# Kernel optimization log

Measured on AMD Instinct MI355X. Metric: run time of the kernel, lower is better.

## Reference

```python
import jax, jax.numpy as jnp
import numpy as np

B, F, V, E, H, D = 1024, 2048, 10000, 256, 512, 3


def setup_inputs() -> dict:
    key = jax.random.key(0)
    ks = jax.random.split(key, 16)
    n = lambda k, shape, s: (jax.random.normal(k, shape, dtype=jnp.float32) * s)
    fz = lambda shape: jnp.zeros(shape, jnp.float32)
    forget_bias = fz((4 * H,)).at[H:2 * H].set(1.0)  # torch init: bias_hh forget gate = 1
    return {
        "target": n(ks[0], (B, F), 1.0),
        "distractors": n(ks[1], (D, B, F), 1.0),
        # Sender params
        "s_W_aff": n(ks[2], (H, F), 0.02), "s_b_aff": fz((H,)),
        "s_W_ih": n(ks[3], (4 * H, E), 0.05), "s_W_hh": n(ks[4], (4 * H, H), 0.05),
        "s_b_ih": fz((4 * H,)), "s_b_hh": forget_bias,
        "s_emb": n(ks[5], (V, E), 0.1),
        "s_W_probs": n(ks[6], (V, H), 0.05), "s_b_probs": fz((V,)),
        # Receiver params
        "r_emb": n(ks[7], (V, E), 0.1),
        "r_W_ih": n(ks[8], (4 * H, E), 0.05), "r_W_hh": n(ks[9], (4 * H, H), 0.05),
        "r_b_ih": fz((4 * H,)), "r_b_hh": forget_bias,
        "r_W_aff": n(ks[10], (F, H), 0.02), "r_b_aff": fz((F,)),
        "start_token_idx": 1,
        "max_sentence_length": 20,
    }


def lstm_cell(x, h, c, W_ih, W_hh, b_ih, b_hh):
    # PyTorch LSTMCell gate order: i, f, g, o
    gates = x @ W_ih.T + b_ih + h @ W_hh.T + b_hh
    i, f, g, o = jnp.split(gates, 4, axis=-1)
    c = jax.nn.sigmoid(f) * c + jax.nn.sigmoid(i) * jnp.tanh(g)
    h = jax.nn.sigmoid(o) * jnp.tanh(c)
    return h, c


def reference(target, distractors, s_W_aff, s_b_aff, s_W_ih, s_W_hh, s_b_ih, s_b_hh,
              s_emb, s_W_probs, s_b_probs, r_emb, r_W_ih, r_W_hh, r_b_ih, r_b_hh,
              r_W_aff, r_b_aff, start_token_idx, max_sentence_length):
    # ---- Sender (greedy eval path of the original module) ----
    h0 = target @ s_W_aff.T + s_b_aff                     # [B,H]
    c0 = jnp.zeros((B, H), target.dtype)
    w0 = s_emb[jnp.full((B,), start_token_idx, jnp.int32)]  # [B,E]

    def send_step(carry, _):
        h, c, w = carry
        h, c = lstm_cell(w, h, c, s_W_ih, s_W_hh, s_b_ih, s_b_hh)
        logits = h @ s_W_probs.T + s_b_probs              # [B,V]
        w_idx = jnp.argmax(logits, axis=-1)               # greedy sample
        lp = jax.nn.log_softmax(logits, axis=-1)[jnp.arange(B), w_idx]
        return (h, c, s_emb[w_idx]), (w_idx, lp)

    (_, _, _), (msg_tb, lp_tb) = jax.lax.scan(send_step, (h0, c0, w0), None,
                                              length=max_sentence_length)
    message = msg_tb.T                                    # [B,T]
    log_prob = lp_tb[-1]                                  # log prob of last token, [B]

    # ---- Receiver ----
    def recv_step(carry, w_idx):
        h, c = carry
        h, c = lstm_cell(r_emb[w_idx], h, c, r_W_ih, r_W_hh, r_b_ih, r_b_hh)
        return (h, c), None

    (hr, _), _ = jax.lax.scan(recv_step,
                              (jnp.zeros((B, H), target.dtype), jnp.zeros((B, H), target.dtype)),
                              msg_tb)
    r_transform = hr @ r_W_aff.T + r_b_aff                # [B,F]

    # ---- Hinge loss + accuracy ----
    rT = r_transform.T                                    # [F,B]
    target_score = target @ rT                            # [B,B]
    d_scores = jnp.einsum('dbf,fn->dbn', distractors, rT) # [D,B,B]
    hinge = jnp.sum(jnp.maximum(0.0, 1.0 - target_score[None] + d_scores), axis=0)  # [B,B]
    loss = jnp.mean(jnp.mean(-hinge * log_prob, axis=1))  # log_prob broadcasts over last dim

    target_prob = jnp.mean(jnp.exp(target_score), axis=1)            # [B]
    dist_prob = jnp.mean(jnp.exp(d_scores), axis=2)                  # [D,B]
    all_probs = jnp.concatenate([target_prob[:, None], dist_prob.T], axis=1)  # [B,1+D]
    accuracy = jnp.mean((jnp.argmax(all_probs, axis=1) == 0).astype(jnp.float32))
    return loss, accuracy, message
```

## Files before the change

kernel.cpp:

```cpp
#include <hip/hip_runtime.h>
#include <math.h>
#include <limits.h>

#define NB 1024
#define NF 2048
#define NV 10000
#define NE 256
#define NH 512
#define ND 3
#define NT 20

typedef __bf16 bf16x8 __attribute__((ext_vector_type(8)));
typedef float  f32x4  __attribute__((ext_vector_type(4)));

__device__ __forceinline__ float sigf(float x) { return 1.0f / (1.0f + expf(-x)); }
__device__ __forceinline__ bool better(float v, int i, float w, int j) {
    return (v > w) || (v == w && i < j);
}

template<int ACCUM, int BIAS, int ZMODE>
__global__ __launch_bounds__(256)
void gemm_nt128(const float* __restrict__ A, const float* __restrict__ A2,
                const float* __restrict__ Bm, const float* __restrict__ bias,
                float* __restrict__ C, int M, int N, int K)
{
    __shared__ float As[16][68];
    __shared__ float Bs[16][132];
    const int tid = threadIdx.x;
    const int bn = blockIdx.x << 7;
    const int bm = blockIdx.y << 6;

    const float* Ause = A;
    if (ZMODE) {
        if (blockIdx.z > 0) Ause = A2 + (size_t)(blockIdx.z - 1) * M * K;
        C += (size_t)blockIdx.z * M * N;
    }

    const int sar = tid & 63;
    const int sak = (tid >> 6) << 2;
    const int sbr = tid >> 1;
    const int sbk = (tid & 1) << 3;
    const int tx = tid & 15, ty = tid >> 4;
    const int m0 = ty << 2, n0 = tx << 3;

    float acc[4][8];
    #pragma unroll
    for (int i = 0; i < 4; ++i)
        #pragma unroll
        for (int j = 0; j < 8; ++j) acc[i][j] = 0.f;

    for (int k0 = 0; k0 < K; k0 += 16) {
        float4 av = *(const float4*)(Ause + (size_t)(bm + sar) * K + k0 + sak);
        float4 b0 = *(const float4*)(Bm + (size_t)(bn + sbr) * K + k0 + sbk);
        float4 b1 = *(const float4*)(Bm + (size_t)(bn + sbr) * K + k0 + sbk + 4);
        As[sak + 0][sar] = av.x; As[sak + 1][sar] = av.y;
        As[sak + 2][sar] = av.z; As[sak + 3][sar] = av.w;
        Bs[sbk + 0][sbr] = b0.x; Bs[sbk + 1][sbr] = b0.y;
        Bs[sbk + 2][sbr] = b0.z; Bs[sbk + 3][sbr] = b0.w;
        Bs[sbk + 4][sbr] = b1.x; Bs[sbk + 5][sbr] = b1.y;
        Bs[sbk + 6][sbr] = b1.z; Bs[sbk + 7][sbr] = b1.w;
        __syncthreads();
        #pragma unroll
        for (int k = 0; k < 16; ++k) {
            float4 xa = *(const float4*)&As[k][m0];
            float4 xb0 = *(const float4*)&Bs[k][n0];
            float4 xb1 = *(const float4*)&Bs[k][n0 + 4];
            float ar[4] = {xa.x, xa.y, xa.z, xa.w};
            float br[8] = {xb0.x, xb0.y, xb0.z, xb0.w, xb1.x, xb1.y, xb1.z, xb1.w};
            #pragma unroll
            for (int i = 0; i < 4; ++i)
                #pragma unroll
                for (int j = 0; j < 8; ++j)
                    acc[i][j] = fmaf(ar[i], br[j], acc[i][j]);
        }
        __syncthreads();
    }
    #pragma unroll
    for (int i = 0; i < 4; ++i) {
        int row = bm + m0 + i;
        #pragma unroll
        for (int j = 0; j < 8; ++j) {
            int col = bn + n0 + j;
            float v = acc[i][j];
            if (BIAS) v += bias[col];
            float* p = C + (size_t)row * N + col;
            if (ACCUM) v += *p;
            *p = v;
        }
    }
}

__global__ void split_k(const float* __restrict__ x, __bf16* __restrict__ hi,
                        __bf16* __restrict__ lo, int n)
{
    int i = blockIdx.x * 256 + threadIdx.x;
    if (i < n) {
        float v = x[i];
        __bf16 h = (__bf16)v;
        hi[i] = h;
        lo[i] = (__bf16)(v - (float)h);
    }
}

__global__ __launch_bounds__(256)
void logits_mfma(const __bf16* __restrict__ Ahi, const __bf16* __restrict__ Alo,
                 const __bf16* __restrict__ Bhi, const __bf16* __restrict__ Blo,
                 const float* __restrict__ bias, float* __restrict__ C)
{
    __shared__ __align__(16) char sm[32768];
    __bf16* sAh = (__bf16*)sm;
    __bf16* sAl = (__bf16*)(sm + 8192);
    __bf16* sBh = (__bf16*)(sm + 16384);
    __bf16* sBl = (__bf16*)(sm + 24576);

    const int tid = threadIdx.x;
    const int lane = tid & 63, w = tid >> 6;
    const int wm = w >> 1, wn = w & 1;
    const int bm = blockIdx.y << 7, bn = blockIdx.x << 7;

    size_t ga[2], gb[2];
    #pragma unroll
    for (int j = 0; j < 2; ++j) {
        int s = tid + j * 256;
        int mf = s >> 6, g = (s >> 4) & 3, row = s & 15;
        ga[j] = (size_t)(bm + mf * 16 + row) * NH + g * 8;
        int n = bn + mf * 16 + row;
        if (n >= NV) n = 0;
        gb[j] = (size_t)n * NH + g * 8;
    }

    f32x4 acc[4][4];
    #pragma unroll
    for (int i = 0; i < 4; ++i)
        #pragma unroll
        for (int j = 0; j < 4; ++j) acc[i][j] = (f32x4){0.f, 0.f, 0.f, 0.f};

    for (int k0 = 0; k0 < NH; k0 += 32) {
        uint4 vah0 = *(const uint4*)(Ahi + ga[0] + k0);
        uint4 vah1 = *(const uint4*)(Ahi + ga[1] + k0);
        uint4 val0 = *(const uint4*)(Alo + ga[0] + k0);
        uint4 val1 = *(const uint4*)(Alo + ga[1] + k0);
        uint4 vbh0 = *(const uint4*)(Bhi + gb[0] + k0);
        uint4 vbh1 = *(const uint4*)(Bhi + gb[1] + k0);
        uint4 vbl0 = *(const uint4*)(Blo + gb[0] + k0);
        uint4 vbl1 = *(const uint4*)(Blo + gb[1] + k0);
        *(uint4*)(sAh + (size_t)tid * 8)         = vah0;
        *(uint4*)(sAh + (size_t)(tid + 256) * 8) = vah1;
        *(uint4*)(sAl + (size_t)tid * 8)         = val0;
        *(uint4*)(sAl + (size_t)(tid + 256) * 8) = val1;
        *(uint4*)(sBh + (size_t)tid * 8)         = vbh0;
        *(uint4*)(sBh + (size_t)(tid + 256) * 8) = vbh1;
        *(uint4*)(sBl + (size_t)tid * 8)         = vbl0;
        *(uint4*)(sBl + (size_t)(tid + 256) * 8) = vbl1;
        __syncthreads();

        bf16x8 ah[4], al[4];
        #pragma unroll
        for (int f = 0; f < 4; ++f) {
            int base = ((wm * 4 + f) * 64 + lane) * 8;
            ah[f] = *(const bf16x8*)(sAh + base);
            al[f] = *(const bf16x8*)(sAl + base);
        }
        #pragma unroll
        for (int fn = 0; fn < 4; ++fn) {
            int base = ((wn * 4 + fn) * 64 + lane) * 8;
            bf16x8 bh = *(const bf16x8*)(sBh + base);
            bf16x8 bl = *(const bf16x8*)(sBl + base);
            #pragma unroll
            for (int fm = 0; fm < 4; ++fm)
                acc[fm][fn] = __builtin_amdgcn_mfma_f32_16x16x32_bf16(ah[fm], bh, acc[fm][fn], 0, 0, 0);
            #pragma unroll
            for (int fm = 0; fm < 4; ++fm)
                acc[fm][fn] = __builtin_amdgcn_mfma_f32_16x16x32_bf16(ah[fm], bl, acc[fm][fn], 0, 0, 0);
            #pragma unroll
            for (int fm = 0; fm < 4; ++fm)
                acc[fm][fn] = __builtin_amdgcn_mfma_f32_16x16x32_bf16(al[fm], bh, acc[fm][fn], 0, 0, 0);
        }
        __syncthreads();
    }

    const int r4 = (lane >> 4) << 2, cc = lane & 15;
    #pragma unroll
    for (int fm = 0; fm < 4; ++fm) {
        int row = bm + (wm * 4 + fm) * 16 + r4;
        #pragma unroll
        for (int fn = 0; fn < 4; ++fn) {
            int col = bn + (wn * 4 + fn) * 16 + cc;
            if (col < NV) {
                float bv = bias[col];
                #pragma unroll
                for (int r = 0; r < 4; ++r)
                    C[(size_t)(row + r) * NV + col] = acc[fm][fn][r] + bv;
            }
        }
    }
}

__global__ __launch_bounds__(256)
void lstm_cell_k(const float* __restrict__ gates, float* __restrict__ h, float* __restrict__ c)
{
    int idx = blockIdx.x * 256 + threadIdx.x;
    int b = idx >> 9;
    int j = idx & (NH - 1);
    const float* g = gates + (size_t)b * (4 * NH);
    float gi = sigf(g[j]);
    float gf = sigf(g[NH + j]);
    float gg = tanhf(g[2 * NH + j]);
    float go = sigf(g[3 * NH + j]);
    float cn = gf * c[idx] + gi * gg;
    c[idx] = cn;
    h[idx] = go * tanhf(cn);
}

template<int LAST>
__global__ __launch_bounds__(256)
void argmax2_k(const float* __restrict__ logits, int* __restrict__ top2i,
               float* __restrict__ lse)
{
    __shared__ float sv1[256], sv2[256];
    __shared__ int   si1[256], si2[256];
    const int b = blockIdx.x;
    const int tid = threadIdx.x;
    const float* L = logits + (size_t)b * NV;
    float v1 = -INFINITY, v2 = -INFINITY;
    int i1 = INT_MAX, i2 = INT_MAX;
    for (int v = tid; v < NV; v += 256) {
        float x = L[v];
        if (better(x, v, v1, i1)) { v2 = v1; i2 = i1; v1 = x; i1 = v; }
        else if (better(x, v, v2, i2)) { v2 = x; i2 = v; }
    }
    sv1[tid] = v1; si1[tid] = i1; sv2[tid] = v2; si2[tid] = i2;
    __syncthreads();
    for (int s = 128; s > 0; s >>= 1) {
        if (tid < s) {
            float a1 = sv1[tid], a2 = sv2[tid];     int ai1 = si1[tid], ai2 = si2[tid];
            float b1 = sv1[tid+s], b2 = sv2[tid+s]; int bi1 = si1[tid+s], bi2 = si2[tid+s];
            float r1v, r2v; int r1i, r2i;
            if (better(a1, ai1, b1, bi1)) {
                r1v = a1; r1i = ai1;
                if (better(b1, bi1, a2, ai2)) { r2v = b1; r2i = bi1; }
                else                          { r2v = a2; r2i = ai2; }
            } else {
                r1v = b1; r1i = bi1;
                if (better(a1, ai1, b2, bi2)) { r2v = a1; r2i = ai1; }
                else                          { r2v = b2; r2i = bi2; }
            }
            sv1[tid] = r1v; si1[tid] = r1i; sv2[tid] = r2v; si2[tid] = r2i;
        }
        __syncthreads();
    }
    if (tid == 0) { top2i[2*b] = si1[0]; top2i[2*b+1] = si2[0]; }
    if (LAST) {
        float m = sv1[0];
        __syncthreads();
        float s = 0.0f;
        for (int v = tid; v < NV; v += 256) s += expf(L[v] - m);
        sv1[tid] = s;
        __syncthreads();
        for (int sh = 128; sh > 0; sh >>= 1) {
            if (tid < sh) sv1[tid] += sv1[tid + sh];
            __syncthreads();
        }
        if (tid == 0) lse[b] = m + logf(sv1[0]);
    }
}

template<int LAST>
__global__ __launch_bounds__(64)
void rescore_k(const float* __restrict__ h, const float* __restrict__ Wpr,
               const float* __restrict__ bpr, const float* __restrict__ logits,
               const int* __restrict__ top2i, const float* __restrict__ lse,
               int* __restrict__ msg_t, float* __restrict__ out_msg,
               float* __restrict__ lp, int t)
{
    const int b = blockIdx.x;
    const int tid = threadIdx.x;
    const int i1 = top2i[2*b], i2 = top2i[2*b+1];
    const float* hr = h + (size_t)b * NH;
    const float* w1 = Wpr + (size_t)i1 * NH;
    const float* w2 = Wpr + (size_t)i2 * NH;
    double s1 = 0.0, s2 = 0.0;
    for (int k = tid; k < NH; k += 64) {
        double hv = (double)hr[k];
        s1 += hv * (double)w1[k];
        s2 += hv * (double)w2[k];
    }
    #pragma unroll
    for (int off = 32; off > 0; off >>= 1) {
        s1 += __shfl_down(s1, off);
        s2 += __shfl_down(s2, off);
    }
    if (tid == 0) {
        s1 += (double)bpr[i1];
        s2 += (double)bpr[i2];
        int w = (s1 > s2 || (s1 == s2 && i1 < i2)) ? i1 : i2;
        msg_t[b] = w;
        out_msg[(size_t)b * NT + t] = (float)w;
        if (LAST) lp[b] = logits[(size_t)b * NV + w] - lse[b];
    }
}

__global__ void gather_emb_k(const float* __restrict__ emb, const int* __restrict__ idx,
                             float* __restrict__ x)
{
    int b = blockIdx.x;
    int tok = idx[b];
    const float4* src = (const float4*)(emb + (size_t)tok * NE);
    float4* dst = (float4*)(x + (size_t)b * NE);
    dst[threadIdx.x] = src[threadIdx.x];
}

__global__ void init_idx_k(const int* __restrict__ start, int* __restrict__ idx)
{
    int b = blockIdx.x * 256 + threadIdx.x;
    if (b < NB) idx[b] = start[0];
}

__global__ void bias_comb_k(const float* __restrict__ a, const float* __restrict__ b,
                            float* __restrict__ o)
{
    int n = blockIdx.x * 256 + threadIdx.x;
    if (n < 4 * NH) o[n] = a[n] + b[n];
}

__global__ __launch_bounds__(256)
void loss_row_k(const float* __restrict__ scores, const float* __restrict__ lp,
                float* __restrict__ hsum, float* __restrict__ accb)
{
    __shared__ float red[256];
    const int b = blockIdx.x;
    const int tid = threadIdx.x;
    const float* ts = scores + (size_t)b * NB;
    const float* d0 = scores + (size_t)NB * NB * 1 + (size_t)b * NB;
    const float* d1 = scores + (size_t)NB * NB * 2 + (size_t)b * NB;
    const float* d2 = scores + (size_t)NB * NB * 3 + (size_t)b * NB;
    float hs = 0.f, t0 = 0.f, s0 = 0.f, s1 = 0.f, s2 = 0.f;
    for (int n = tid; n < NB; n += 256) {
        float tv = ts[n], a = d0[n], bb = d1[n], cc = d2[n];
        float hinge_bn = fmaxf(0.f, 1.f - tv + a) + fmaxf(0.f, 1.f - tv + bb)
                       + fmaxf(0.f, 1.f - tv + cc);
        hs += hinge_bn * (-lp[n]);
        t0 += expf(tv); s0 += expf(a); s1 += expf(bb); s2 += expf(cc);
    }
    float vals[5] = {hs, t0, s0, s1, s2};
    float outv[5];
    for (int i = 0; i < 5; ++i) {
        red[tid] = vals[i]; __syncthreads();
        for (int s = 128; s > 0; s >>= 1) {
            if (tid < s) red[tid] += red[tid + s];
            __syncthreads();
        }
        outv[i] = red[0]; __syncthreads();
    }
    if (tid == 0) {
        hsum[b] = outv[0];
        accb[b] = (outv[1] >= outv[2] && outv[1] >= outv[3] && outv[1] >= outv[4]) ? 1.0f : 0.0f;
    }
}

__global__ __launch_bounds__(256)
void loss_final_k(const float* __restrict__ hsum, const float* __restrict__ accb,
                  float* __restrict__ out)
{
    __shared__ float red[256];
    const int tid = threadIdx.x;
    float s = 0.f, a = 0.f;
    for (int b = tid; b < NB; b += 256) { s += hsum[b]; a += accb[b]; }
    red[tid] = s; __syncthreads();
    for (int sh = 128; sh > 0; sh >>= 1) { if (tid < sh) red[tid] += red[tid + sh]; __syncthreads(); }
    s = red[0]; __syncthreads();
    red[tid] = a; __syncthreads();
    for (int sh = 128; sh > 0; sh >>= 1) { if (tid < sh) red[tid] += red[tid + sh]; __syncthreads(); }
    a = red[0];
    if (tid == 0) {
        out[0] = s / (float)((size_t)NB * NB);
        out[1] = a / (float)NB;
    }
}

extern "C" void kernel_launch(void* const* d_in, const int* in_sizes, int n_in,
                              void* d_out, int out_size, void* d_ws, size_t ws_size,
                              hipStream_t stream)
{
    const float* target   = (const float*)d_in[0];
    const float* distract = (const float*)d_in[1];
    const float* sWaff = (const float*)d_in[2];
    const float* sbaff = (const float*)d_in[3];
    const float* sWih  = (const float*)d_in[4];
    const float* sWhh  = (const float*)d_in[5];
    const float* sbih  = (const float*)d_in[6];
    const float* sbhh  = (const float*)d_in[7];
    const float* semb  = (const float*)d_in[8];
    const float* sWpr  = (const float*)d_in[9];
    const float* sbpr  = (const float*)d_in[10];
    const float* remb  = (const float*)d_in[11];
    const float* rWih  = (const float*)d_in[12];
    const float* rWhh  = (const float*)d_in[13];
    const float* rbih  = (const float*)d_in[14];
    const float* rbhh  = (const float*)d_in[15];
    const float* rWaff = (const float*)d_in[16];
    const float* rbaff = (const float*)d_in[17];
    const int*   start = (const int*)d_in[18];
    (void)in_sizes; (void)n_in; (void)out_size; (void)ws_size;

    float* out = (float*)d_out;
    float* ws  = (float*)d_ws;

    size_t o = 0;
    float* logits = ws + o; o += (size_t)NB * NV;
    float* gates  = ws + o; o += (size_t)NB * 4 * NH;
    float* xbuf   = ws + o; o += (size_t)NB * NE;
    float* h_s    = ws + o; o += (size_t)NB * NH;
    float* c_s    = ws + o; o += (size_t)NB * NH;
    float* h_r    = ws + o; o += (size_t)NB * NH;
    float* c_r    = ws + o; o += (size_t)NB * NH;
    float* lp     = ws + o; o += NB;
    float* lse    = ws + o; o += NB;
    float* bias_s = ws + o; o += 4 * NH;
    float* bias_r = ws + o; o += 4 * NH;
    float* hsum   = ws + o; o += NB;
    float* accb   = ws + o; o += NB;
    int* msg      = (int*)(ws + o); o += (size_t)NB * NT;
    int* idx0     = (int*)(ws + o); o += NB;
    int* top2i    = (int*)(ws + o); o += 2 * NB;
    __bf16* WHi   = (__bf16*)(ws + o); o += (size_t)NV * NH / 2;
    __bf16* WLo   = (__bf16*)(ws + o); o += (size_t)NV * NH / 2;
    __bf16* hHi   = (__bf16*)(ws + o); o += (size_t)NB * NH / 2;
    __bf16* hLo   = (__bf16*)(ws + o); o += (size_t)NB * NH / 2;

    bias_comb_k<<<8, 256, 0, stream>>>(sbih, sbhh, bias_s);
    bias_comb_k<<<8, 256, 0, stream>>>(rbih, rbhh, bias_r);
    init_idx_k<<<4, 256, 0, stream>>>(start, idx0);
    hipMemsetAsync(c_s, 0, (size_t)NB * NH * 4, stream);
    hipMemsetAsync(h_r, 0, (size_t)NB * NH * 4, stream);
    hipMemsetAsync(c_r, 0, (size_t)NB * NH * 4, stream);

    split_k<<<(NV * NH + 255) / 256, 256, 0, stream>>>(sWpr, WHi, WLo, NV * NH);

    gemm_nt128<0,1,0><<<dim3(NH/128, NB/64), 256, 0, stream>>>(
        target, nullptr, sWaff, sbaff, h_s, NB, NH, NF);

    const int* cur = idx0;
    for (int t = 0; t < NT; ++t) {
        gather_emb_k<<<NB, 64, 0, stream>>>(semb, cur, xbuf);
        gemm_nt128<0,1,0><<<dim3(4*NH/128, NB/64), 256, 0, stream>>>(
            xbuf, nullptr, sWih, bias_s, gates, NB, 4*NH, NE);
        gemm_nt128<1,0,0><<<dim3(4*NH/128, NB/64), 256, 0, stream>>>(
            h_s, nullptr, sWhh, nullptr, gates, NB, 4*NH, NH);
        lstm_cell_k<<<NB*NH/256, 256, 0, stream>>>(gates, h_s, c_s);
        split_k<<<(NB * NH + 255) / 256, 256, 0, stream>>>(h_s, hHi, hLo, NB * NH);
        logits_mfma<<<dim3((NV + 127) / 128, NB / 128), 256, 0, stream>>>(
            hHi, hLo, WHi, WLo, sbpr, logits);
        if (t == NT - 1) {
            argmax2_k<1><<<NB, 256, 0, stream>>>(logits, top2i, lse);
            rescore_k<1><<<NB, 64, 0, stream>>>(h_s, sWpr, sbpr, logits, top2i, lse,
                                                msg + (size_t)t*NB, out + 2, lp, t);
        } else {
            argmax2_k<0><<<NB, 256, 0, stream>>>(logits, top2i, lse);
            rescore_k<0><<<NB, 64, 0, stream>>>(h_s, sWpr, sbpr, logits, top2i, lse,
                                                msg + (size_t)t*NB, out + 2, lp, t);
        }
        cur = msg + (size_t)t * NB;
    }

    for (int t = 0; t < NT; ++t) {
        gather_emb_k<<<NB, 64, 0, stream>>>(remb, msg + (size_t)t*NB, xbuf);
        gemm_nt128<0,1,0><<<dim3(4*NH/128, NB/64), 256, 0, stream>>>(
            xbuf, nullptr, rWih, bias_r, gates, NB, 4*NH, NE);
        gemm_nt128<1,0,0><<<dim3(4*NH/128, NB/64), 256, 0, stream>>>(
            h_r, nullptr, rWhh, nullptr, gates, NB, 4*NH, NH);
        lstm_cell_k<<<NB*NH/256, 256, 0, stream>>>(gates, h_r, c_r);
    }

    float* rtr = gates;
    gemm_nt128<0,1,0><<<dim3(NF/128, NB/64), 256, 0, stream>>>(
        h_r, nullptr, rWaff, rbaff, rtr, NB, NF, NH);

    float* scores = logits;
    gemm_nt128<0,0,1><<<dim3(NB/128, NB/64, 1 + ND), 256, 0, stream>>>(
        target, distract, rtr, nullptr, scores, NB, NB, NF);

    loss_row_k<<<NB, 256, 0, stream>>>(scores, lp, hsum, accb);
    loss_final_k<<<1, 256, 0, stream>>>(hsum, accb, out);
}
```

Before: 6.106 ms.

## Fuse embedding gather, hi/lo split and receiver gate GEMMs; use 512-thread GEMM tiles

```diff
diff --git a/kernel.cpp b/kernel.cpp
--- a/kernel.cpp
+++ b/kernel.cpp
@@ -18,11 +18,12 @@
     return (v > w) || (v == w && i < j);
 }
 
-template<int ACCUM, int BIAS, int ZMODE>
-__global__ __launch_bounds__(256)
-void gemm_nt128(const float* __restrict__ A, const float* __restrict__ A2,
-                const float* __restrict__ Bm, const float* __restrict__ bias,
-                float* __restrict__ C, int M, int N, int K)
+template<int ACCUM, int BIAS, int ZMODE, int GATHER>
+__global__ __launch_bounds__(512)
+void gemm512(const float* __restrict__ A, const float* __restrict__ A2,
+             const int* __restrict__ gidx,
+             const float* __restrict__ Bm, const float* __restrict__ bias,
+             float* __restrict__ C, int M, int N, int K)
 {
     __shared__ float As[16][68];
     __shared__ float Bs[16][132];
@@ -36,41 +37,46 @@
         C += (size_t)blockIdx.z * M * N;
     }
 
-    const int sar = tid & 63;
-    const int sak = (tid >> 6) << 2;
-    const int sbr = tid >> 1;
-    const int sbk = (tid & 1) << 3;
-    const int tx = tid & 15, ty = tid >> 4;
-    const int m0 = ty << 2, n0 = tx << 3;
-
-    float acc[4][8];
+    const int abr = tid & 63;
+    const int abk = ((tid >> 6) & 3) << 2;
+    const int bbr = tid & 127;
+    const int bbk = (tid >> 7) << 2;
+    const int tx = tid & 31, ty = tid >> 5;
+    const int m0 = ty << 2, n0 = tx << 2;
+
+    const float* Arow = nullptr;
+    if (tid < 256) {
+        int r = bm + abr;
+        Arow = GATHER ? (A + (size_t)gidx[r] * K) : (Ause + (size_t)r * K);
+    }
+    const float* Brow = Bm + (size_t)(bn + bbr) * K;
+
+    float acc[4][4];
     #pragma unroll
     for (int i = 0; i < 4; ++i)
         #pragma unroll
-        for (int j = 0; j < 8; ++j) acc[i][j] = 0.f;
+        for (int j = 0; j < 4; ++j) acc[i][j] = 0.f;
 
     for (int k0 = 0; k0 < K; k0 += 16) {
-        float4 av = *(const float4*)(Ause + (size_t)(bm + sar) * K + k0 + sak);
-        float4 b0 = *(const float4*)(Bm + (size_t)(bn + sbr) * K + k0 + sbk);
-        float4 b1 = *(const float4*)(Bm + (size_t)(bn + sbr) * K + k0 + sbk + 4);
-        As[sak + 0][sar] = av.x; As[sak + 1][sar] = av.y;
-        As[sak + 2][sar] = av.z; As[sak + 3][sar] = av.w;
-        Bs[sbk + 0][sbr] = b0.x; Bs[sbk + 1][sbr] = b0.y;
-        Bs[sbk + 2][sbr] = b0.z; Bs[sbk + 3][sbr] = b0.w;
-        Bs[sbk + 4][sbr] = b1.x; Bs[sbk + 5][sbr] = b1.y;
-        Bs[sbk + 6][sbr] = b1.z; Bs[sbk + 7][sbr] = b1.w;
+        if (tid < 256) {
+            float4 av = *(const float4*)(Arow + k0 + abk);
+            As[abk + 0][abr] = av.x; As[abk + 1][abr] = av.y;
+            As[abk + 2][abr] = av.z; As[abk + 3][abr] = av.w;
+        }
+        float4 bv = *(const float4*)(Brow + k0 + bbk);
+        Bs[bbk + 0][bbr] = bv.x; Bs[bbk + 1][bbr] = bv.y;
+        Bs[bbk + 2][bbr] = bv.z; Bs[bbk + 3][bbr] = bv.w;
         __syncthreads();
         #pragma unroll
         for (int k = 0; k < 16; ++k) {
             float4 xa = *(const float4*)&As[k][m0];
-            float4 xb0 = *(const float4*)&Bs[k][n0];
-            float4 xb1 = *(const float4*)&Bs[k][n0 + 4];
+            float4 xb = *(const float4*)&Bs[k][n0];
             float ar[4] = {xa.x, xa.y, xa.z, xa.w};
-            float br[8] = {xb0.x, xb0.y, xb0.z, xb0.w, xb1.x, xb1.y, xb1.z, xb1.w};
+            float br[4] = {xb.x, xb.y, xb.z, xb.w};
             #pragma unroll
             for (int i = 0; i < 4; ++i)
                 #pragma unroll
-                for (int j = 0; j < 8; ++j)
+                for (int j = 0; j < 4; ++j)
                     acc[i][j] = fmaf(ar[i], br[j], acc[i][j]);
         }
         __syncthreads();
@@ -79,13 +85,84 @@
     for (int i = 0; i < 4; ++i) {
         int row = bm + m0 + i;
         #pragma unroll
-        for (int j = 0; j < 8; ++j) {
+        for (int j = 0; j < 4; ++j) {
             int col = bn + n0 + j;
             float v = acc[i][j];
             if (BIAS) v += bias[col];
             float* p = C + (size_t)row * N + col;
             if (ACCUM) v += *p;
             *p = v;
+        }
+    }
+}
+
+__global__ __launch_bounds__(512)
+void recv_gate_k(const float* __restrict__ emb, const int* __restrict__ msg_t,
+                 const float* __restrict__ h, const float* __restrict__ Wih,
+                 const float* __restrict__ Whh, const float* __restrict__ bias,
+                 float* __restrict__ gates)
+{
+    __shared__ float As[16][68];
+    __shared__ float Bs[16][132];
+    const int tid = threadIdx.x;
+    const int bn = blockIdx.x << 7;
+    const int bm = blockIdx.y << 6;
+
+    const int abr = tid & 63;
+    const int abk = ((tid >> 6) & 3) << 2;
+    const int bbr = tid & 127;
+    const int bbk = (tid >> 7) << 2;
+    const int tx = tid & 31, ty = tid >> 5;
+    const int m0 = ty << 2, n0 = tx << 2;
+
+    const float* Ax = nullptr; const float* Ah = nullptr;
+    if (tid < 256) {
+        int r = bm + abr;
+        Ax = emb + (size_t)msg_t[r] * NE;
+        Ah = h + (size_t)r * NH;
+    }
+    const float* Bi = Wih + (size_t)(bn + bbr) * NE;
+    const float* Bh = Whh + (size_t)(bn + bbr) * NH;
+
+    float acc[4][4];
+    #pragma unroll
+    for (int i = 0; i < 4; ++i)
+        #pragma unroll
+        for (int j = 0; j < 4; ++j) acc[i][j] = 0.f;
+
+    for (int k0 = 0; k0 < NE + NH; k0 += 16) {
+        if (tid < 256) {
+            float4 av = (k0 < NE) ? *(const float4*)(Ax + k0 + abk)
+                                  : *(const float4*)(Ah + (k0 - NE) + abk);
+            As[abk + 0][abr] = av.x; As[abk + 1][abr] = av.y;
+            As[abk + 2][abr] = av.z; As[abk + 3][abr] = av.w;
+        }
+        float4 bv = (k0 < NE) ? *(const float4*)(Bi + k0 + bbk)
+                              : *(const float4*)(Bh + (k0 - NE) + bbk);
+        Bs[bbk + 0][bbr] = bv.x; Bs[bbk + 1][bbr] = bv.y;
+        Bs[bbk + 2][bbr] = bv.z; Bs[bbk + 3][bbr] = bv.w;
+        __syncthreads();
+        #pragma unroll
+        for (int k = 0; k < 16; ++k) {
+            float4 xa = *(const float4*)&As[k][m0];
+            float4 xb = *(const float4*)&Bs[k][n0];
+            float ar[4] = {xa.x, xa.y, xa.z, xa.w};
+            float br[4] = {xb.x, xb.y, xb.z, xb.w};
+            #pragma unroll
+            for (int i = 0; i < 4; ++i)
+                #pragma unroll
+                for (int j = 0; j < 4; ++j)
+                    acc[i][j] = fmaf(ar[i], br[j], acc[i][j]);
+        }
+        __syncthreads();
+    }
+    #pragma unroll
+    for (int i = 0; i < 4; ++i) {
+        int row = bm + m0 + i;
+        #pragma unroll
+        for (int j = 0; j < 4; ++j) {
+            int col = bn + n0 + j;
+            gates[(size_t)row * (4 * NH) + col] = acc[i][j] + bias[col];
         }
     }
 }
@@ -196,8 +273,11 @@
     }
 }
 
+template<int SPLIT>
 __global__ __launch_bounds__(256)
-void lstm_cell_k(const float* __restrict__ gates, float* __restrict__ h, float* __restrict__ c)
+void lstm_cell_k(const float* __restrict__ gates, float* __restrict__ h,
+                 float* __restrict__ c, __bf16* __restrict__ hi,
+                 __bf16* __restrict__ lo)
 {
     int idx = blockIdx.x * 256 + threadIdx.x;
     int b = idx >> 9;
@@ -209,7 +289,13 @@
     float go = sigf(g[3 * NH + j]);
     float cn = gf * c[idx] + gi * gg;
     c[idx] = cn;
-    h[idx] = go * tanhf(cn);
+    float hv = go * tanhf(cn);
+    h[idx] = hv;
+    if (SPLIT) {
+        __bf16 hb = (__bf16)hv;
+        hi[idx] = hb;
+        lo[idx] = (__bf16)(hv - (float)hb);
+    }
 }
 
 template<int LAST>
@@ -298,16 +384,6 @@
         out_msg[(size_t)b * NT + t] = (float)w;
         if (LAST) lp[b] = logits[(size_t)b * NV + w] - lse[b];
     }
-}
-
-__global__ void gather_emb_k(const float* __restrict__ emb, const int* __restrict__ idx,
-                             float* __restrict__ x)
-{
-    int b = blockIdx.x;
-    int tok = idx[b];
-    const float4* src = (const float4*)(emb + (size_t)tok * NE);
-    float4* dst = (float4*)(x + (size_t)b * NE);
-    dst[threadIdx.x] = src[threadIdx.x];
 }
 
 __global__ void init_idx_k(const int* __restrict__ start, int* __restrict__ idx)
@@ -427,6 +503,7 @@
     __bf16* WLo   = (__bf16*)(ws + o); o += (size_t)NV * NH / 2;
     __bf16* hHi   = (__bf16*)(ws + o); o += (size_t)NB * NH / 2;
     __bf16* hLo   = (__bf16*)(ws + o); o += (size_t)NB * NH / 2;
+    (void)xbuf;
 
     bias_comb_k<<<8, 256, 0, stream>>>(sbih, sbhh, bias_s);
     bias_comb_k<<<8, 256, 0, stream>>>(rbih, rbhh, bias_r);
@@ -437,18 +514,16 @@
 
     split_k<<<(NV * NH + 255) / 256, 256, 0, stream>>>(sWpr, WHi, WLo, NV * NH);
 
-    gemm_nt128<0,1,0><<<dim3(NH/128, NB/64), 256, 0, stream>>>(
-        target, nullptr, sWaff, sbaff, h_s, NB, NH, NF);
+    gemm512<0,1,0,0><<<dim3(NH/128, NB/64), 512, 0, stream>>>(
+        target, nullptr, nullptr, sWaff, sbaff, h_s, NB, NH, NF);
 
     const int* cur = idx0;
     for (int t = 0; t < NT; ++t) {
-        gather_emb_k<<<NB, 64, 0, stream>>>(semb, cur, xbuf);
-        gemm_nt128<0,1,0><<<dim3(4*NH/128, NB/64), 256, 0, stream>>>(
-            xbuf, nullptr, sWih, bias_s, gates, NB, 4*NH, NE);
-        gemm_nt128<1,0,0><<<dim3(4*NH/128, NB/64), 256, 0, stream>>>(
-            h_s, nullptr, sWhh, nullptr, gates, NB, 4*NH, NH);
-        lstm_cell_k<<<NB*NH/256, 256, 0, stream>>>(gates, h_s, c_s);
-        split_k<<<(NB * NH + 255) / 256, 256, 0, stream>>>(h_s, hHi, hLo, NB * NH);
+        gemm512<0,1,0,1><<<dim3(4*NH/128, NB/64), 512, 0, stream>>>(
+            semb, nullptr, cur, sWih, bias_s, gates, NB, 4*NH, NE);
+        gemm512<1,0,0,0><<<dim3(4*NH/128, NB/64), 512, 0, stream>>>(
+            h_s, nullptr, nullptr, sWhh, nullptr, gates, NB, 4*NH, NH);
+        lstm_cell_k<1><<<NB*NH/256, 256, 0, stream>>>(gates, h_s, c_s, hHi, hLo);
         logits_mfma<<<dim3((NV + 127) / 128, NB / 128), 256, 0, stream>>>(
             hHi, hLo, WHi, WLo, sbpr, logits);
         if (t == NT - 1) {
@@ -464,21 +539,18 @@
     }
 
     for (int t = 0; t < NT; ++t) {
-        gather_emb_k<<<NB, 64, 0, stream>>>(remb, msg + (size_t)t*NB, xbuf);
-        gemm_nt128<0,1,0><<<dim3(4*NH/128, NB/64), 256, 0, stream>>>(
-            xbuf, nullptr, rWih, bias_r, gates, NB, 4*NH, NE);
-        gemm_nt128<1,0,0><<<dim3(4*NH/128, NB/64), 256, 0, stream>>>(
-            h_r, nullptr, rWhh, nullptr, gates, NB, 4*NH, NH);
-        lstm_cell_k<<<NB*NH/256, 256, 0, stream>>>(gates, h_r, c_r);
+        recv_gate_k<<<dim3(4*NH/128, NB/64), 512, 0, stream>>>(
+            remb, msg + (size_t)t*NB, h_r, rWih, rWhh, bias_r, gates);
+        lstm_cell_k<0><<<NB*NH/256, 256, 0, stream>>>(gates, h_r, c_r, nullptr, nullptr);
     }
 
     float* rtr = gates;
-    gemm_nt128<0,1,0><<<dim3(NF/128, NB/64), 256, 0, stream>>>(
-        h_r, nullptr, rWaff, rbaff, rtr, NB, NF, NH);
+    gemm512<0,1,0,0><<<dim3(NF/128, NB/64), 512, 0, stream>>>(
+        h_r, nullptr, nullptr, rWaff, rbaff, rtr, NB, NF, NH);
 
     float* scores = logits;
-    gemm_nt128<0,0,1><<<dim3(NB/128, NB/64, 1 + ND), 256, 0, stream>>>(
-        target, distract, rtr, nullptr, scores, NB, NB, NF);
+    gemm512<0,0,1,0><<<dim3(NB/128, NB/64, 1 + ND), 512, 0, stream>>>(
+        target, distract, nullptr, rtr, nullptr, scores, NB, NB, NF);
 
     loss_row_k<<<NB, 256, 0, stream>>>(scores, lp, hsum, accb);
     loss_final_k<<<1, 256, 0, stream>>>(hsum, accb, out);
```

After: 5.386 ms. -11.8%, faster.
